# Kernel tuning notes

Hardware: AMD Instinct MI355X
Metric: run time of the kernel (lower is better)

Reference implementation:

```python
import jax, jax.numpy as jnp
import numpy as np
import math

B, T, C, NH = 4, 2048, 1024, 16
D = C // NH  # 64, rotary_dim == D

def _rope_tables():
    inv_freq = 1.0 / (10000.0 ** (np.arange(0, D, 2, dtype=np.float32) / D))
    t = np.arange(T, dtype=np.float32)
    freqs = np.outer(t, inv_freq)                 # [T, D/2]
    emb = np.concatenate([freqs, freqs], axis=-1)  # [T, D]
    return jnp.asarray(np.cos(emb))[None], jnp.asarray(np.sin(emb))[None]  # [1,T,D]

def setup_inputs() -> dict:
    key = jax.random.key(0)
    ks = jax.random.split(key, 3)
    x = jax.random.normal(ks[0], (B, T, C), dtype=jnp.float32)
    w_attn = jax.random.normal(ks[1], (3 * C, C), dtype=jnp.float32) * (1.0 / math.sqrt(C))
    b_attn = jnp.zeros((3 * C,), dtype=jnp.float32)
    w_proj = jax.random.normal(ks[2], (C, C), dtype=jnp.float32) * (1.0 / math.sqrt(C))
    b_proj = jnp.zeros((C,), dtype=jnp.float32)
    cos, sin = _rope_tables()
    return {"x": x, "w_attn": w_attn, "b_attn": b_attn,
            "w_proj": w_proj, "b_proj": b_proj, "cos": cos, "sin": sin}

def _rotate_half(u):
    u1, u2 = jnp.split(u, 2, axis=-1)
    return jnp.concatenate([-u2, u1], axis=-1)

def reference(x, w_attn, b_attn, w_proj, b_proj, cos, sin):
    Bx, Tx, Cx = x.shape
    nh, d = NH, Cx // NH
    # fused QKV projection (torch Linear: y = x @ W^T + b)
    qkv = x @ w_attn.T + b_attn                      # [B,T,3C]
    q, k, v = jnp.split(qkv, 3, axis=-1)
    q = q.reshape(Bx, Tx, nh, d).transpose(0, 2, 1, 3)  # [B,nh,T,d]
    k = k.reshape(Bx, Tx, nh, d).transpose(0, 2, 1, 3)
    v = v.reshape(Bx, Tx, nh, d).transpose(0, 2, 1, 3)
    # RoPE (rotary_dim == d, full head)
    c = cos[:, None, :, :]  # [1,1,T,d]
    s = sin[:, None, :, :]
    q = q * c + _rotate_half(q) * s
    k = k * c + _rotate_half(k) * s
    # naive causal attention
    scores = jnp.einsum("bhqd,bhkd->bhqk", q, k) / math.sqrt(d)
    causal = jnp.tril(jnp.ones((Tx, Tx), dtype=bool))
    scores = jnp.where(causal[None, None], scores, -jnp.inf)
    att = jax.nn.softmax(scores, axis=-1)
    y = jnp.einsum("bhqk,bhkd->bhqd", att, v)        # [B,nh,T,d]
    y = y.transpose(0, 2, 1, 3).reshape(Bx, Tx, Cx)
    return y @ w_proj.T + b_proj
```

## Files before the change

### kernel.cpp

```cpp
#include <hip/hip_runtime.h>

typedef __bf16 bf16_t;
typedef bf16_t bf16x8 __attribute__((ext_vector_type(8)));
typedef bf16_t bf16x4 __attribute__((ext_vector_type(4)));
typedef float f32x4 __attribute__((ext_vector_type(4)));

constexpr int BATCH = 4, SEQ = 2048, CH = 1024, NHEAD = 16, HD = 64;
constexpr int BM = 128, BN = 128, BKK = 64;

#define LGKM_FENCE() __asm__ __volatile__("s_waitcnt lgkmcnt(0)" ::: "memory")
#define VM_FENCE() __asm__ __volatile__("s_waitcnt vmcnt(0)" ::: "memory")

__device__ __forceinline__ void g2lds16(const bf16_t* g, bf16_t* l) {
  __builtin_amdgcn_global_load_lds((__attribute__((address_space(1))) void*)(g),
                                   (__attribute__((address_space(3))) void*)(l),
                                   16, 0, 0);
}

__device__ __forceinline__ f32x4 mfma16(bf16x8 a, bf16x8 b, f32x4 c) {
  return __builtin_amdgcn_mfma_f32_16x16x32_bf16(a, b, c, 0, 0, 0);
}

__global__ __launch_bounds__(256) void cvt3_kernel(const float4* __restrict__ x,
                                                   ushort4* __restrict__ dx,
                                                   const float4* __restrict__ wa,
                                                   ushort4* __restrict__ dwa,
                                                   const float4* __restrict__ wp,
                                                   ushort4* __restrict__ dwp) {
  int bid = blockIdx.x;
  const float4* s;
  ushort4* d;
  int i;
  if (bid < 8192) {
    s = x; d = dx; i = bid * 256 + threadIdx.x;
  } else if (bid < 11264) {
    s = wa; d = dwa; i = (bid - 8192) * 256 + threadIdx.x;
  } else {
    s = wp; d = dwp; i = (bid - 11264) * 256 + threadIdx.x;
  }
  float4 f = s[i];
  ushort4 o;
  o.x = __builtin_bit_cast(unsigned short, (bf16_t)f.x);
  o.y = __builtin_bit_cast(unsigned short, (bf16_t)f.y);
  o.z = __builtin_bit_cast(unsigned short, (bf16_t)f.z);
  o.w = __builtin_bit_cast(unsigned short, (bf16_t)f.w);
  d[i] = o;
}

__device__ __forceinline__ void gemm_mainloop(const bf16_t* __restrict__ A,
                                              const bf16_t* __restrict__ W, int Kdim,
                                              int m0, int n0,
                                              bf16_t* As, bf16_t* Bs,
                                              f32x4 acc[4][4]) {
  const int tid = threadIdx.x;
  const int lane = tid & 63;
  const int w = tid >> 6;
  const int quad = lane >> 4, l16 = lane & 15;
  const int wm = (w >> 1) << 6, wn = (w & 1) << 6;
  const int srow = tid >> 3;
  const int scol = ((tid & 7) ^ (srow & 7)) << 3;
  const int dcol = (tid & 7) << 3;
  const int key = l16 & 15 & 7;
  const bf16_t* ga[4];
  const bf16_t* gb[4];
  bf16_t *la[4], *lb[4];
#pragma unroll
  for (int p = 0; p < 4; p++) {
    int row = p * 32 + srow;
    ga[p] = A + (size_t)(m0 + row) * Kdim + scol;
    gb[p] = W + (size_t)(n0 + row) * Kdim + scol;
    la[p] = As + row * BKK + dcol;
    lb[p] = Bs + row * BKK + dcol;
  }
  for (int k0 = 0; k0 < Kdim; k0 += BKK) {
#pragma unroll
    for (int p = 0; p < 4; p++) g2lds16(ga[p] + k0, la[p]);
#pragma unroll
    for (int p = 0; p < 4; p++) g2lds16(gb[p] + k0, lb[p]);
    VM_FENCE();
    __syncthreads();
#pragma unroll
    for (int ki = 0; ki < 2; ki++) {
      bf16x8 av[4], bv[4];
#pragma unroll
      for (int i = 0; i < 4; i++)
        av[i] = *(const bf16x8*)&As[(wm + i * 16 + l16) * BKK +
                                    ((((ki << 2) | quad) ^ key) << 3)];
#pragma unroll
      for (int i = 0; i < 4; i++)
        bv[i] = *(const bf16x8*)&Bs[(wn + i * 16 + l16) * BKK +
                                    ((((ki << 2) | quad) ^ key) << 3)];
#pragma unroll
      for (int mi = 0; mi < 4; mi++)
#pragma unroll
        for (int ni = 0; ni < 4; ni++)
          acc[mi][ni] = mfma16(av[mi], bv[ni], acc[mi][ni]);
    }
    __syncthreads();
  }
}

constexpr float SCL = 0.125f * 1.44269504089f;

__global__ __launch_bounds__(256) void qkv_rope_kernel(
    const bf16_t* __restrict__ X, const bf16_t* __restrict__ Wa,
    const float* __restrict__ ba, const float* __restrict__ cosT,
    const float* __restrict__ sinT, bf16_t* __restrict__ Q,
    bf16_t* __restrict__ Ko, bf16_t* __restrict__ VT) {
  constexpr int TSTRIDE = 68;
  __shared__ __align__(16) char smem[4 * 64 * TSTRIDE * 2];
  bf16_t* As = (bf16_t*)smem;
  bf16_t* Bs = As + BM * BKK;

  f32x4 acc[4][4];
#pragma unroll
  for (int i = 0; i < 4; i++)
#pragma unroll
    for (int j = 0; j < 4; j++) acc[i][j] = (f32x4){0.f, 0.f, 0.f, 0.f};

  const int id = blockIdx.x;
  const int sid = ((id & 7) * 192) + (id >> 3);
  const int n0 = (sid % 24) * BN;
  const int m0 = (sid / 24) * BM;
  gemm_mainloop(X, Wa, CH, m0, n0, As, Bs, acc);

  const int tid = threadIdx.x, lane = tid & 63, w = tid >> 6;
  const int quad = lane >> 4, l16 = lane & 15;
  const int wm = (w >> 1) << 6, wn = (w & 1) << 6;
  const int nbase = n0 + wn;
  const int part = nbase >> 10;
  const int h = (nbase & 1023) >> 6;
  const int mbase = m0 + wm;
  const int bb = mbase >> 11;
  const size_t headbase = ((size_t)(bb * NHEAD + h)) * SEQ * HD;

  if (part < 2) {
    bf16_t* O = (part == 0) ? Q : Ko;
    const float post = (part == 0) ? SCL : 1.0f;
#pragma unroll
    for (int mi = 0; mi < 4; mi++)
#pragma unroll
      for (int r = 0; r < 4; r++) {
        int m = mbase + mi * 16 + quad * 4 + r;
        int t = m & (SEQ - 1);
        const float* cr = cosT + t * HD;
        const float* sr = sinT + t * HD;
        size_t rowo = headbase + (size_t)t * HD;
#pragma unroll
        for (int ni = 0; ni < 2; ni++) {
          int d0 = ni * 16 + l16, d1 = d0 + 32;
          float v0 = acc[mi][ni][r] + ba[nbase + d0];
          float v1 = acc[mi][ni + 2][r] + ba[nbase + d1];
          float r0 = (v0 * cr[d0] - v1 * sr[d0]) * post;
          float r1 = (v1 * cr[d1] + v0 * sr[d1]) * post;
          O[rowo + d0] = (bf16_t)r0;
          O[rowo + d1] = (bf16_t)r1;
        }
      }
  } else {
    bf16_t* tb = (bf16_t*)smem + w * 64 * TSTRIDE;
    int t0 = mbase & (SEQ - 1);
#pragma unroll
    for (int mi = 0; mi < 4; mi++)
#pragma unroll
      for (int ni = 0; ni < 4; ni++) {
        int d = ni * 16 + l16;
        float bias = ba[nbase + d];
#pragma unroll
        for (int r = 0; r < 4; r++) {
          float v = acc[mi][ni][r] + bias;
          tb[d * TSTRIDE + mi * 16 + quad * 4 + r] = (bf16_t)v;
        }
      }
    LGKM_FENCE();
    int half = lane >> 5, l5 = lane & 31;
    size_t vbase = ((size_t)(bb * NHEAD + h)) * HD * SEQ;
#pragma unroll
    for (int it = 0; it < 32; it++) {
      int d = it * 2 + half;
      unsigned int val = *(const unsigned int*)&tb[d * TSTRIDE + l5 * 2];
      *(unsigned int*)&VT[vbase + (size_t)d * SEQ + t0 + l5 * 2] = val;
    }
  }
}

__device__ __forceinline__ void sm_update(f32x4 (&s)[4], float& lr,
                                          bf16_t* Prow, int quad,
                                          int swz, bool domask, int lim) {
  if (domask) {
#pragma unroll
    for (int ni = 0; ni < 4; ni++)
#pragma unroll
      for (int r = 0; r < 4; r++)
        if (ni * 16 + r > lim) s[ni][r] = -1e30f;
  }
  float sum = 0.f;
#pragma unroll
  for (int ni = 0; ni < 4; ni++) {
    float p0 = __builtin_exp2f(s[ni][0]);
    float p1 = __builtin_exp2f(s[ni][1]);
    float p2 = __builtin_exp2f(s[ni][2]);
    float p3 = __builtin_exp2f(s[ni][3]);
    bf16x4 pk = {(bf16_t)p0, (bf16_t)p1, (bf16_t)p2, (bf16_t)p3};
    *(bf16x4*)&Prow[(((ni << 2) | quad) ^ (swz << 1)) << 2] = pk;
    sum += (p0 + p1) + (p2 + p3);
  }
  lr += sum;
}

__global__ __launch_bounds__(256) void flash_kernel(const bf16_t* __restrict__ Q,
                                                    const bf16_t* __restrict__ Kg,
                                                    const bf16_t* __restrict__ VT,
                                                    bf16_t* __restrict__ att) {
  __shared__ __align__(16) bf16_t Ks[2][64 * 64];
  __shared__ __align__(16) bf16_t Vs[2][64 * 64];
  __shared__ __align__(16) bf16_t Pt[4][16 * 64];
  const int tid = threadIdx.x, w = tid >> 6, lane = tid & 63;
  const int quad = lane >> 4, l16 = lane & 15;
  const int p = (int)blockIdx.x >> 6;
  const int bh = (int)blockIdx.x & 63;
  const bf16_t* Qp = Q + (size_t)bh * SEQ * HD;
  const bf16_t* Kb = Kg + (size_t)bh * SEQ * HD;
  const bf16_t* Vb = VT + (size_t)bh * HD * SEQ;
  const int grow = lane >> 3;
  const int gj8 = ((lane & 7) ^ grow) * 8;
  const int i0 = w * 2;
  const int sw = l16 & 7;
  const int swz = l16 >> 1;
  const int bloc = bh >> 4, hh = bh & 15;
  bf16_t* Pw = &Pt[w][l16 * 64];
  const int rs0 = (quad ^ swz) << 3;
  const int rs1 = ((4 + quad) ^ swz) << 3;

  auto stage = [&](int kcs, int b) {
#pragma unroll
    for (int ii = 0; ii < 2; ii++) {
      int i = i0 + ii;
      g2lds16(Kb + (size_t)(kcs + i * 8 + grow) * HD + gj8, &Ks[b][(i * 64 + lane) * 8]);
      g2lds16(Vb + (size_t)(i * 8 + grow) * SEQ + kcs + gj8, &Vs[b][(i * 64 + lane) * 8]);
    }
  };

  for (int sp = 0; sp < 2; ++sp) {
    const int j = sp ? p : 31 - p;
    const int m = j * 64 + w * 16;
    const int nch = j + 1;
    bf16x8 aq0 = *(const bf16x8*)&Qp[(size_t)(m + l16) * HD + quad * 8];
    bf16x8 aq1 = *(const bf16x8*)&Qp[(size_t)(m + l16) * HD + 32 + quad * 8];
    float lr = 0.f;
    f32x4 y[4];
#pragma unroll
    for (int ni = 0; ni < 4; ni++) y[ni] = (f32x4){0.f, 0.f, 0.f, 0.f};

    stage(0, 0);
    VM_FENCE();
    __syncthreads();

    for (int c = 0; c < nch; ++c) {
      const int kc = c * 64, buf = c & 1;
      if (c + 1 < nch) stage(kc + 64, buf ^ 1);
      f32x4 s[4];
#pragma unroll
      for (int ni = 0; ni < 4; ni++) {
        bf16x8 k0 = *(const bf16x8*)&Ks[buf][((ni * 16 + l16) * 8 + (quad ^ sw)) * 8];
        bf16x8 k1 = *(const bf16x8*)&Ks[buf][((ni * 16 + l16) * 8 + ((4 + quad) ^ sw)) * 8];
        f32x4 z = (f32x4){0.f, 0.f, 0.f, 0.f};
        s[ni] = mfma16(k1, aq1, mfma16(k0, aq0, z));
      }
      sm_update(s, lr, Pw, quad, swz, c == nch - 1, m + l16 - kc - quad * 4);
      LGKM_FENCE();
      bf16x8 p0 = *(const bf16x8*)&Pw[rs0];
      bf16x8 p1 = *(const bf16x8*)&Pw[rs1];
#pragma unroll
      for (int ni = 0; ni < 4; ni++) {
        bf16x8 v0 = *(const bf16x8*)&Vs[buf][((ni * 16 + l16) * 8 + (quad ^ sw)) * 8];
        bf16x8 v1 = *(const bf16x8*)&Vs[buf][((ni * 16 + l16) * 8 + ((4 + quad) ^ sw)) * 8];
        y[ni] = mfma16(v1, p1, mfma16(v0, p0, y[ni]));
      }
      VM_FENCE();
      __syncthreads();
    }

    lr += __shfl_xor(lr, 16);
    lr += __shfl_xor(lr, 32);
    float inv = 1.f / lr;
    size_t rb = ((size_t)bloc * SEQ + m + l16) * CH + hh * HD + quad * 4;
#pragma unroll
    for (int ni = 0; ni < 4; ni++) {
      bf16x4 o = {(bf16_t)(y[ni][0] * inv), (bf16_t)(y[ni][1] * inv),
                  (bf16_t)(y[ni][2] * inv), (bf16_t)(y[ni][3] * inv)};
      *(bf16x4*)&att[rb + ni * 16] = o;
    }
  }
}

__global__ __launch_bounds__(256) void proj_kernel(const bf16_t* __restrict__ A,
                                                   const bf16_t* __restrict__ Wp,
                                                   const float* __restrict__ bp,
                                                   float* __restrict__ out) {
  __shared__ __align__(16) bf16_t As[BM * BKK];
  __shared__ __align__(16) bf16_t Bs[BN * BKK];
  f32x4 acc[4][4];
#pragma unroll
  for (int i = 0; i < 4; i++)
#pragma unroll
    for (int j = 0; j < 4; j++) acc[i][j] = (f32x4){0.f, 0.f, 0.f, 0.f};
  const int id = blockIdx.x;
  const int sid = ((id & 7) * 64) + (id >> 3);
  const int n0 = (sid % 8) * BN;
  const int m0 = (sid / 8) * BM;
  gemm_mainloop(A, Wp, CH, m0, n0, As, Bs, acc);
  const int tid = threadIdx.x, lane = tid & 63, w = tid >> 6;
  const int quad = lane >> 4, l16 = lane & 15;
  const int wm = (w >> 1) << 6, wn = (w & 1) << 6;
  const int nbase = n0 + wn, mbase = m0 + wm;
#pragma unroll
  for (int mi = 0; mi < 4; mi++)
#pragma unroll
    for (int r = 0; r < 4; r++) {
      int m = mbase + mi * 16 + quad * 4 + r;
#pragma unroll
      for (int ni = 0; ni < 4; ni++) {
        int n = nbase + ni * 16 + l16;
        out[(size_t)m * CH + n] = acc[mi][ni][r] + bp[n];
      }
    }
}

extern "C" void kernel_launch(void* const* d_in, const int* in_sizes, int n_in,
                              void* d_out, int out_size, void* d_ws, size_t ws_size,
                              hipStream_t stream) {
  const float* x      = (const float*)d_in[0];
  const float* w_attn = (const float*)d_in[1];
  const float* b_attn = (const float*)d_in[2];
  const float* w_proj = (const float*)d_in[3];
  const float* b_proj = (const float*)d_in[4];
  const float* cosT   = (const float*)d_in[5];
  const float* sinT   = (const float*)d_in[6];
  float* out = (float*)d_out;

  bf16_t* xbf  = (bf16_t*)d_ws;
  bf16_t* wabf = xbf + (size_t)8192 * 1024;
  bf16_t* wpbf = wabf + (size_t)3072 * 1024;
  bf16_t* Qb   = wpbf + (size_t)1024 * 1024;
  bf16_t* Kb   = Qb + (size_t)8388608;
  bf16_t* VTb  = Kb + (size_t)8388608;
  bf16_t* attb = VTb + (size_t)8388608;

  cvt3_kernel<<<12288, 256, 0, stream>>>((const float4*)x, (ushort4*)xbf,
                                         (const float4*)w_attn, (ushort4*)wabf,
                                         (const float4*)w_proj, (ushort4*)wpbf);
  qkv_rope_kernel<<<dim3(1536), 256, 0, stream>>>(xbf, wabf, b_attn, cosT, sinT,
                                                  Qb, Kb, VTb);
  flash_kernel<<<dim3(1024), 256, 0, stream>>>(Qb, Kb, VTb, attb);
  proj_kernel<<<dim3(512), 256, 0, stream>>>(attb, wpbf, b_proj, out);
}
```

Measured before the change: 266.8 us.

## Compute softmax row sums via MFMA and shrink proj tiles to 64x128

The flash kernel stops summing exponentials with scalar adds and cross-lane shuffles. It instead accumulates the row sum with two extra MFMAs against a vector of ones, reusing the P fragments already loaded. The projection kernel now uses 64x128 tiles with its own inlined mainloop, launching 1024 blocks instead of 512 for better CU occupancy. The trade-off is less data reuse per block in the projection and extra MFMA work per chunk in attention.

```diff
diff --git a/kernel.cpp b/kernel.cpp
--- a/kernel.cpp
+++ b/kernel.cpp
@@ -60,7 +60,7 @@
   const int srow = tid >> 3;
   const int scol = ((tid & 7) ^ (srow & 7)) << 3;
   const int dcol = (tid & 7) << 3;
-  const int key = l16 & 15 & 7;
+  const int key = l16 & 7;
   const bf16_t* ga[4];
   const bf16_t* gb[4];
   bf16_t *la[4], *lb[4];
@@ -184,8 +184,7 @@
   }
 }
 
-__device__ __forceinline__ void sm_update(f32x4 (&s)[4], float& lr,
-                                          bf16_t* Prow, int quad,
+__device__ __forceinline__ void sm_update(f32x4 (&s)[4], bf16_t* Prow, int quad,
                                           int swz, bool domask, int lim) {
   if (domask) {
 #pragma unroll
@@ -194,7 +193,6 @@
       for (int r = 0; r < 4; r++)
         if (ni * 16 + r > lim) s[ni][r] = -1e30f;
   }
-  float sum = 0.f;
 #pragma unroll
   for (int ni = 0; ni < 4; ni++) {
     float p0 = __builtin_exp2f(s[ni][0]);
@@ -203,9 +201,7 @@
     float p3 = __builtin_exp2f(s[ni][3]);
     bf16x4 pk = {(bf16_t)p0, (bf16_t)p1, (bf16_t)p2, (bf16_t)p3};
     *(bf16x4*)&Prow[(((ni << 2) | quad) ^ (swz << 1)) << 2] = pk;
-    sum += (p0 + p1) + (p2 + p3);
-  }
-  lr += sum;
+  }
 }
 
 __global__ __launch_bounds__(256) void flash_kernel(const bf16_t* __restrict__ Q,
@@ -232,6 +228,9 @@
   const int rs0 = (quad ^ swz) << 3;
   const int rs1 = ((4 + quad) ^ swz) << 3;
 
+  const bf16x8 ones = {(bf16_t)1.f, (bf16_t)1.f, (bf16_t)1.f, (bf16_t)1.f,
+                       (bf16_t)1.f, (bf16_t)1.f, (bf16_t)1.f, (bf16_t)1.f};
+
   auto stage = [&](int kcs, int b) {
 #pragma unroll
     for (int ii = 0; ii < 2; ii++) {
@@ -247,8 +246,8 @@
     const int nch = j + 1;
     bf16x8 aq0 = *(const bf16x8*)&Qp[(size_t)(m + l16) * HD + quad * 8];
     bf16x8 aq1 = *(const bf16x8*)&Qp[(size_t)(m + l16) * HD + 32 + quad * 8];
-    float lr = 0.f;
     f32x4 y[4];
+    f32x4 sum_acc = (f32x4){0.f, 0.f, 0.f, 0.f};
 #pragma unroll
     for (int ni = 0; ni < 4; ni++) y[ni] = (f32x4){0.f, 0.f, 0.f, 0.f};
 
@@ -267,10 +266,11 @@
         f32x4 z = (f32x4){0.f, 0.f, 0.f, 0.f};
         s[ni] = mfma16(k1, aq1, mfma16(k0, aq0, z));
       }
-      sm_update(s, lr, Pw, quad, swz, c == nch - 1, m + l16 - kc - quad * 4);
+      sm_update(s, Pw, quad, swz, c == nch - 1, m + l16 - kc - quad * 4);
       LGKM_FENCE();
       bf16x8 p0 = *(const bf16x8*)&Pw[rs0];
       bf16x8 p1 = *(const bf16x8*)&Pw[rs1];
+      sum_acc = mfma16(ones, p1, mfma16(ones, p0, sum_acc));
 #pragma unroll
       for (int ni = 0; ni < 4; ni++) {
         bf16x8 v0 = *(const bf16x8*)&Vs[buf][((ni * 16 + l16) * 8 + (quad ^ sw)) * 8];
@@ -281,9 +281,7 @@
       __syncthreads();
     }
 
-    lr += __shfl_xor(lr, 16);
-    lr += __shfl_xor(lr, 32);
-    float inv = 1.f / lr;
+    float inv = 1.f / sum_acc[0];
     size_t rb = ((size_t)bloc * SEQ + m + l16) * CH + hh * HD + quad * 4;
 #pragma unroll
     for (int ni = 0; ni < 4; ni++) {
@@ -298,24 +296,74 @@
                                                    const bf16_t* __restrict__ Wp,
                                                    const float* __restrict__ bp,
                                                    float* __restrict__ out) {
-  __shared__ __align__(16) bf16_t As[BM * BKK];
-  __shared__ __align__(16) bf16_t Bs[BN * BKK];
-  f32x4 acc[4][4];
-#pragma unroll
-  for (int i = 0; i < 4; i++)
+  __shared__ __align__(16) bf16_t As[64 * BKK];
+  __shared__ __align__(16) bf16_t Bs[128 * BKK];
+  f32x4 acc[2][4];
+#pragma unroll
+  for (int i = 0; i < 2; i++)
 #pragma unroll
     for (int j = 0; j < 4; j++) acc[i][j] = (f32x4){0.f, 0.f, 0.f, 0.f};
+
   const int id = blockIdx.x;
-  const int sid = ((id & 7) * 64) + (id >> 3);
-  const int n0 = (sid % 8) * BN;
-  const int m0 = (sid / 8) * BM;
-  gemm_mainloop(A, Wp, CH, m0, n0, As, Bs, acc);
+  const int sid = ((id & 7) * 128) + (id >> 3);
+  const int n0 = (sid % 8) * 128;
+  const int m0 = (sid / 8) * 64;
+
   const int tid = threadIdx.x, lane = tid & 63, w = tid >> 6;
   const int quad = lane >> 4, l16 = lane & 15;
-  const int wm = (w >> 1) << 6, wn = (w & 1) << 6;
+  const int wm = (w >> 1) << 5;
+  const int wn = (w & 1) << 6;
+  const int srow = tid >> 3;
+  const int scol = ((tid & 7) ^ (srow & 7)) << 3;
+  const int dcol = (tid & 7) << 3;
+  const int key = l16 & 7;
+
+  const bf16_t* ga[2];
+  bf16_t* la[2];
+  const bf16_t* gb[4];
+  bf16_t* lb[4];
+#pragma unroll
+  for (int p = 0; p < 2; p++) {
+    int row = p * 32 + srow;
+    ga[p] = A + (size_t)(m0 + row) * CH + scol;
+    la[p] = As + row * BKK + dcol;
+  }
+#pragma unroll
+  for (int p = 0; p < 4; p++) {
+    int row = p * 32 + srow;
+    gb[p] = Wp + (size_t)(n0 + row) * CH + scol;
+    lb[p] = Bs + row * BKK + dcol;
+  }
+  for (int k0 = 0; k0 < CH; k0 += BKK) {
+#pragma unroll
+    for (int p = 0; p < 2; p++) g2lds16(ga[p] + k0, la[p]);
+#pragma unroll
+    for (int p = 0; p < 4; p++) g2lds16(gb[p] + k0, lb[p]);
+    VM_FENCE();
+    __syncthreads();
+#pragma unroll
+    for (int ki = 0; ki < 2; ki++) {
+      bf16x8 av[2], bv[4];
+#pragma unroll
+      for (int i = 0; i < 2; i++)
+        av[i] = *(const bf16x8*)&As[(wm + i * 16 + l16) * BKK +
+                                    ((((ki << 2) | quad) ^ key) << 3)];
+#pragma unroll
+      for (int i = 0; i < 4; i++)
+        bv[i] = *(const bf16x8*)&Bs[(wn + i * 16 + l16) * BKK +
+                                    ((((ki << 2) | quad) ^ key) << 3)];
+#pragma unroll
+      for (int mi = 0; mi < 2; mi++)
+#pragma unroll
+        for (int ni = 0; ni < 4; ni++)
+          acc[mi][ni] = mfma16(av[mi], bv[ni], acc[mi][ni]);
+    }
+    __syncthreads();
+  }
+
   const int nbase = n0 + wn, mbase = m0 + wm;
 #pragma unroll
-  for (int mi = 0; mi < 4; mi++)
+  for (int mi = 0; mi < 2; mi++)
 #pragma unroll
     for (int r = 0; r < 4; r++) {
       int m = mbase + mi * 16 + quad * 4 + r;
@@ -353,5 +401,5 @@
   qkv_rope_kernel<<<dim3(1536), 256, 0, stream>>>(xbf, wabf, b_attn, cosT, sinT,
                                                   Qb, Kb, VTb);
   flash_kernel<<<dim3(1024), 256, 0, stream>>>(Qb, Kb, VTb, attb);
-  proj_kernel<<<dim3(512), 256, 0, stream>>>(attb, wpbf, b_proj, out);
-}
+  proj_kernel<<<dim3(1024), 256, 0, stream>>>(attb, wpbf, b_proj, out);
+}
```

Measured after the change: 264.8 us. About the same (-0.7%).
